# Optimization experiments

Measured on AMD Instinct MI355X. Metric: run time of the kernel, lower is better.

Reference implementation:

```python
import jax, jax.numpy as jnp
import numpy as np

N_HEADS = 16

def setup_inputs() -> dict:
    key = jax.random.key(0)
    qkv = jax.random.normal(key, (4, 3072, 2048), dtype=jnp.float32)
    return {"qkv": qkv}

def reference(qkv) -> jnp.ndarray:
    bs, width, length = qkv.shape
    ch = width // (3 * N_HEADS)
    # [bs*H, 3*ch, T] -> split into q, k, v each [bs*H, ch, T]
    qkv_r = qkv.reshape(bs * N_HEADS, 3 * ch, length)
    q, k, v = qkv_r[:, :ch], qkv_r[:, ch:2 * ch], qkv_r[:, 2 * ch:]
    scale = 1.0 / jnp.sqrt(jnp.sqrt(jnp.float32(ch)))
    # scores: [bs*H, T, T]
    weight = jnp.einsum('bct,bcs->bts', q * scale, k * scale)
    weight = jax.nn.softmax(weight.astype(jnp.float32), axis=-1).astype(weight.dtype)
    a = jnp.einsum('bts,bcs->bct', weight, v)  # [bs*H, ch, T]
    return a.reshape(bs, N_HEADS * ch, length)
```

## Files before the change

### kernel.cpp

```cpp
#include <hip/hip_runtime.h>

namespace {

constexpr int D  = 64;
constexpr int T  = 2048;
constexpr int TQ = 64;
constexpr int NT = T / 64;
constexpr float SCL = 0.125f * 1.44269504088896340736f;

constexpr size_t QP_OFF  = (size_t)64 * 32 * 8192;
constexpr size_t WS_NEED = ((size_t)64 * 32 * 8192 + (size_t)64 * 32 * 4096) * 2;

typedef __bf16 bf16x8 __attribute__((ext_vector_type(8)));
typedef float  f32x4  __attribute__((ext_vector_type(4)));
typedef unsigned short u16x4 __attribute__((ext_vector_type(4)));

__device__ inline unsigned short f2bf(float f) {
    unsigned int u = __builtin_bit_cast(unsigned int, f);
    u += 0x7FFFu + ((u >> 16) & 1u);
    return (unsigned short)(u >> 16);
}

__device__ inline bf16x8 frag8(const unsigned short* p, int row, int c0) {
    int g = (c0 >> 3) ^ ((row >> 1) & 7);
    return *(const bf16x8*)(p + row * 64 + g * 8);
}

__device__ inline void async_cp16(const void* g, void* l) {
    __builtin_amdgcn_global_load_lds(
        (const __attribute__((address_space(1))) unsigned int*)g,
        (__attribute__((address_space(3))) unsigned int*)l, 16, 0, 0);
}

__global__ __launch_bounds__(256)
void prepass(const float* __restrict__ qkv, unsigned short* __restrict__ ws) {
    const int tile = blockIdx.x, h = blockIdx.y, z = blockIdx.z;
    const int tid = threadIdx.x;
    const int c0 = (tid >> 4) * 4;
    const int s4 = tid & 15;
    const float* src = qkv + (size_t)h * 3 * D * T + (size_t)z * D * T + tile * 64;
    unsigned short* dst = (z == 0)
        ? ws + QP_OFF + (size_t)(h * 32 + tile) * 4096
        : ws + (size_t)(h * 32 + tile) * 8192 + (z == 2 ? 4096 : 0);

    float fr[4][4];
    #pragma unroll
    for (int r = 0; r < 4; r++)
        *(f32x4*)fr[r] = *(const f32x4*)(src + (size_t)(c0 + r) * T + s4 * 4);

    if (z < 2) {
        #pragma unroll
        for (int j = 0; j < 4; j++) {
            int trow = s4 * 4 + j;
            int g = (c0 >> 3) ^ ((trow >> 1) & 7);
            u16x4 w = { f2bf(fr[0][j]), f2bf(fr[1][j]), f2bf(fr[2][j]), f2bf(fr[3][j]) };
            *(u16x4*)(dst + trow * 64 + g * 8 + (c0 & 7)) = w;
        }
    } else {
        #pragma unroll
        for (int r = 0; r < 4; r++) {
            int row = c0 + r, cc = s4 * 4;
            int g = (cc >> 3) ^ ((row >> 1) & 7);
            u16x4 w = { f2bf(fr[r][0]), f2bf(fr[r][1]), f2bf(fr[r][2]), f2bf(fr[r][3]) };
            *(u16x4*)(dst + row * 64 + g * 8 + (cc & 7)) = w;
        }
    }
}

__global__ __launch_bounds__(256, 4)
void attn_main(const unsigned short* __restrict__ ws, float* __restrict__ out) {
    const int h  = blockIdx.x;
    const int qt = blockIdx.y;
    const int t0 = qt * TQ;
    const int tid  = threadIdx.x;
    const int lane = tid & 63;
    const int w    = tid >> 6;
    const int sh   = w & 1, th = w >> 1;
    const int ln   = lane & 15, q4 = lane >> 4;

    __shared__ unsigned short KV[2][8192];
    __shared__ unsigned short Ps[4096];

    const unsigned short* qtile = ws + QP_OFF + (size_t)(h * 32 + qt) * 4096;
    bf16x8 bQ[2][2];
    #pragma unroll
    for (int ti = 0; ti < 2; ti++)
        #pragma unroll
        for (int kc = 0; kc < 2; kc++) {
            int t = th * 32 + ti * 16 + ln;
            int g = (kc * 4 + q4) ^ ((t >> 1) & 7);
            bQ[ti][kc] = *(const bf16x8*)(qtile + t * 64 + g * 8);
        }

    const char* kvbase = (const char*)ws + (size_t)(h * 32) * 16384
                         + (size_t)w * 4096 + lane * 16;
    {
        char* l = (char*)&KV[0][0] + w * 4096;
        #pragma unroll
        for (int i = 0; i < 4; i++) async_cp16(kvbase + i * 1024, l + i * 1024);
    }

    f32x4 acc_o[4][2];
    #pragma unroll
    for (int ci = 0; ci < 4; ci++)
        #pragma unroll
        for (int ti = 0; ti < 2; ti++) acc_o[ci][ti] = (f32x4){0.f, 0.f, 0.f, 0.f};
    float l_acc[2] = {0.f, 0.f};

    for (int kt = 0; kt < NT; kt++) {
        const int buf = kt & 1;
        __syncthreads();
        if (kt + 1 < NT) {
            const char* g = kvbase + (size_t)(kt + 1) * 16384;
            char* l = (char*)&KV[buf ^ 1][0] + w * 4096;
            #pragma unroll
            for (int i = 0; i < 4; i++) async_cp16(g + i * 1024, l + i * 1024);
        }
        const unsigned short* Kr = &KV[buf][0];
        const unsigned short* Vr = &KV[buf][4096];

        f32x4 acc_s[2][2];
        #pragma unroll
        for (int si = 0; si < 2; si++)
            #pragma unroll
            for (int ti = 0; ti < 2; ti++) acc_s[si][ti] = (f32x4){0.f, 0.f, 0.f, 0.f};
        #pragma unroll
        for (int kc = 0; kc < 2; kc++)
            #pragma unroll
            for (int si = 0; si < 2; si++) {
                bf16x8 aK = frag8(Kr, sh * 32 + si * 16 + ln, kc * 32 + q4 * 8);
                #pragma unroll
                for (int ti = 0; ti < 2; ti++)
                    acc_s[si][ti] = __builtin_amdgcn_mfma_f32_16x16x32_bf16(
                        aK, bQ[ti][kc], acc_s[si][ti], 0, 0, 0);
            }

        #pragma unroll
        for (int si = 0; si < 2; si++)
            #pragma unroll
            for (int ti = 0; ti < 2; ti++) {
                float p0 = __builtin_amdgcn_exp2f(acc_s[si][ti][0] * SCL);
                float p1 = __builtin_amdgcn_exp2f(acc_s[si][ti][1] * SCL);
                float p2 = __builtin_amdgcn_exp2f(acc_s[si][ti][2] * SCL);
                float p3 = __builtin_amdgcn_exp2f(acc_s[si][ti][3] * SCL);
                l_acc[ti] += (p0 + p1) + (p2 + p3);
                u16x4 pk = { f2bf(p0), f2bf(p1), f2bf(p2), f2bf(p3) };
                int t  = th * 32 + ti * 16 + ln;
                int c0 = sh * 32 + si * 16 + q4 * 4;
                int g  = (c0 >> 3) ^ ((t >> 1) & 7);
                *(u16x4*)(Ps + t * 64 + g * 8 + (c0 & 7)) = pk;
            }

        bf16x8 bP[2];
        #pragma unroll
        for (int ti = 0; ti < 2; ti++)
            bP[ti] = frag8(Ps, th * 32 + ti * 16 + ln, sh * 32 + q4 * 8);
        #pragma unroll
        for (int ci = 0; ci < 4; ci++) {
            bf16x8 aV = frag8(Vr, ci * 16 + ln, sh * 32 + q4 * 8);
            #pragma unroll
            for (int ti = 0; ti < 2; ti++)
                acc_o[ci][ti] = __builtin_amdgcn_mfma_f32_16x16x32_bf16(
                    aV, bP[ti], acc_o[ci][ti], 0, 0, 0);
        }
    }

    __syncthreads();
    float* mrg = (float*)&KV[0][0];
    float* lp  = (float*)Ps;
    #pragma unroll
    for (int ti = 0; ti < 2; ti++) {
        float s = l_acc[ti];
        s += __shfl_xor(s, 16, 64);
        s += __shfl_xor(s, 32, 64);
        if (q4 == 0) lp[th * 64 + sh * 32 + ti * 16 + ln] = s;
    }
    if (sh == 0) {
        float* base = mrg + th * 2048;
        #pragma unroll
        for (int ci = 0; ci < 4; ci++)
            #pragma unroll
            for (int ti = 0; ti < 2; ti++)
                *(f32x4*)(base + (ci * 2 + ti) * 256 + lane * 4) = acc_o[ci][ti];
    }
    __syncthreads();
    if (sh == 1) {
        float* base = mrg + th * 2048;
        float linv[2];
        #pragma unroll
        for (int ti = 0; ti < 2; ti++) {
            int tt = ti * 16 + ln;
            linv[ti] = 1.0f / (lp[th * 64 + tt] + lp[th * 64 + 32 + tt]);
        }
        float* ob = out + (size_t)h * D * T + t0 + th * 32;
        #pragma unroll
        for (int ci = 0; ci < 4; ci++)
            #pragma unroll
            for (int ti = 0; ti < 2; ti++) {
                f32x4 part = *(const f32x4*)(base + (ci * 2 + ti) * 256 + lane * 4);
                #pragma unroll
                for (int r = 0; r < 4; r++) {
                    int c = ci * 16 + q4 * 4 + r;
                    ob[(size_t)c * T + ti * 16 + ln] =
                        (acc_o[ci][ti][r] + part[r]) * linv[ti];
                }
            }
    }
}

__global__ __launch_bounds__(256)
void attn_fallback(const float* __restrict__ qkv, float* __restrict__ out) {
    const int h     = blockIdx.y;
    const int t0    = blockIdx.x * TQ;
    const int tid   = threadIdx.x;
    const int lane  = tid & 63;
    const int strip = tid >> 6;
    const int ln    = lane & 15;
    const int q4    = lane >> 4;

    __shared__ unsigned short Qs[TQ * D];
    __shared__ unsigned short Ks[64 * D];
    __shared__ unsigned short Vs[D * 64];
    __shared__ unsigned short Pss[TQ * 64];
    __shared__ float l_lds[TQ];

    const float* qb = qkv + (size_t)h * 3 * D * T;
    const float* kb = qb + (size_t)D * T;
    const float* vb = qb + (size_t)(2 * D) * T;
    const int s4 = tid & 15;
    const int c0 = (tid >> 4) * 4;
    {
        float fr[4][4];
        #pragma unroll
        for (int r = 0; r < 4; r++)
            *(f32x4*)fr[r] = *(const f32x4*)(qb + (size_t)(c0 + r) * T + t0 + s4 * 4);
        #pragma unroll
        for (int j = 0; j < 4; j++) {
            int trow = s4 * 4 + j;
            int g = (c0 >> 3) ^ ((trow >> 1) & 7);
            u16x4 wv = { f2bf(fr[0][j]), f2bf(fr[1][j]), f2bf(fr[2][j]), f2bf(fr[3][j]) };
            *(u16x4*)(Qs + trow * 64 + g * 8 + (c0 & 7)) = wv;
        }
    }
    __syncthreads();
    const int arow = strip * 16 + ln;
    const int kg   = q4 * 8;
    const bf16x8 aq0 = frag8(Qs, arow, kg);
    const bf16x8 aq1 = frag8(Qs, arow, 32 + kg);
    f32x4 acc_o[4];
    #pragma unroll
    for (int m = 0; m < 4; m++) acc_o[m] = (f32x4){0.f, 0.f, 0.f, 0.f};
    float l_acc[4] = {0.f, 0.f, 0.f, 0.f};
    for (int kt = 0; kt < NT; kt++) {
        const int s0 = kt * 64;
        float kr[4][4], vr[4][4];
        #pragma unroll
        for (int r = 0; r < 4; r++)
            *(f32x4*)kr[r] = *(const f32x4*)(kb + (size_t)(c0 + r) * T + s0 + s4 * 4);
        #pragma unroll
        for (int r = 0; r < 4; r++)
            *(f32x4*)vr[r] = *(const f32x4*)(vb + (size_t)(c0 + r) * T + s0 + s4 * 4);
        __syncthreads();
        #pragma unroll
        for (int j = 0; j < 4; j++) {
            int srow = s4 * 4 + j;
            int g = (c0 >> 3) ^ ((srow >> 1) & 7);
            u16x4 wk = { f2bf(kr[0][j]), f2bf(kr[1][j]), f2bf(kr[2][j]), f2bf(kr[3][j]) };
            *(u16x4*)(Ks + srow * 64 + g * 8 + (c0 & 7)) = wk;
        }
        #pragma unroll
        for (int r = 0; r < 4; r++) {
            int row = c0 + r, cc = s4 * 4;
            int g = (cc >> 3) ^ ((row >> 1) & 7);
            u16x4 wv = { f2bf(vr[r][0]), f2bf(vr[r][1]), f2bf(vr[r][2]), f2bf(vr[r][3]) };
            *(u16x4*)(Vs + row * 64 + g * 8 + (cc & 7)) = wv;
        }
        __syncthreads();
        f32x4 accs[4];
        #pragma unroll
        for (int ns = 0; ns < 4; ns++) {
            bf16x8 b0 = frag8(Ks, ns * 16 + ln, kg);
            bf16x8 b1 = frag8(Ks, ns * 16 + ln, 32 + kg);
            f32x4 z = {0.f, 0.f, 0.f, 0.f};
            z = __builtin_amdgcn_mfma_f32_16x16x32_bf16(aq0, b0, z, 0, 0, 0);
            z = __builtin_amdgcn_mfma_f32_16x16x32_bf16(aq1, b1, z, 0, 0, 0);
            accs[ns] = z;
        }
        #pragma unroll
        for (int ns = 0; ns < 4; ns++) {
            int scol = ns * 16 + ln;
            #pragma unroll
            for (int r = 0; r < 4; r++) {
                float p = __builtin_amdgcn_exp2f(accs[ns][r] * SCL);
                l_acc[r] += p;
                int trow = strip * 16 + q4 * 4 + r;
                int g = ((scol >> 3) ^ ((trow >> 1) & 7));
                Pss[trow * 64 + g * 8 + (scol & 7)] = f2bf(p);
            }
        }
        bf16x8 bp0 = frag8(Pss, arow, kg);
        bf16x8 bp1 = frag8(Pss, arow, 32 + kg);
        #pragma unroll
        for (int ms = 0; ms < 4; ms++) {
            bf16x8 av0 = frag8(Vs, ms * 16 + ln, kg);
            bf16x8 av1 = frag8(Vs, ms * 16 + ln, 32 + kg);
            acc_o[ms] = __builtin_amdgcn_mfma_f32_16x16x32_bf16(av0, bp0, acc_o[ms], 0, 0, 0);
            acc_o[ms] = __builtin_amdgcn_mfma_f32_16x16x32_bf16(av1, bp1, acc_o[ms], 0, 0, 0);
        }
    }
    #pragma unroll
    for (int r = 0; r < 4; r++) {
        float s = l_acc[r];
        s += __shfl_xor(s, 1, 64);
        s += __shfl_xor(s, 2, 64);
        s += __shfl_xor(s, 4, 64);
        s += __shfl_xor(s, 8, 64);
        if (ln == 0) l_lds[strip * 16 + q4 * 4 + r] = s;
    }
    const float linv = 1.0f / l_lds[strip * 16 + ln];
    const int tg = t0 + strip * 16 + ln;
    float* ob = out + (size_t)h * D * T;
    #pragma unroll
    for (int ms = 0; ms < 4; ms++)
        #pragma unroll
        for (int r = 0; r < 4; r++) {
            int c = ms * 16 + q4 * 4 + r;
            ob[(size_t)c * T + tg] = acc_o[ms][r] * linv;
        }
}

}

extern "C" void kernel_launch(void* const* d_in, const int* in_sizes, int n_in,
                              void* d_out, int out_size, void* d_ws, size_t ws_size,
                              hipStream_t stream) {
    const float* qkv = (const float*)d_in[0];
    float* out = (float*)d_out;
    if (ws_size >= WS_NEED) {
        prepass<<<dim3(32, 64, 3), 256, 0, stream>>>(qkv, (unsigned short*)d_ws);
        attn_main<<<dim3(64, 32), 256, 0, stream>>>((const unsigned short*)d_ws, out);
    } else {
        attn_fallback<<<dim3(32, 64), 256, 0, stream>>>(qkv, out);
    }
}
```

Baseline: 257.7 us.

## Fold softmax scale into Q prepass, precompute LDS pointers, unroll KV loop by two

```diff
diff --git a/kernel.cpp b/kernel.cpp
--- a/kernel.cpp
+++ b/kernel.cpp
@@ -14,6 +14,7 @@
 typedef __bf16 bf16x8 __attribute__((ext_vector_type(8)));
 typedef float  f32x4  __attribute__((ext_vector_type(4)));
 typedef unsigned short u16x4 __attribute__((ext_vector_type(4)));
+typedef unsigned short u16x8 __attribute__((ext_vector_type(8)));
 
 __device__ inline unsigned short f2bf(float f) {
     unsigned int u = __builtin_bit_cast(unsigned int, f);
@@ -21,9 +22,9 @@
     return (unsigned short)(u >> 16);
 }
 
-__device__ inline bf16x8 frag8(const unsigned short* p, int row, int c0) {
+__device__ inline int frag_off(int row, int c0) {
     int g = (c0 >> 3) ^ ((row >> 1) & 7);
-    return *(const bf16x8*)(p + row * 64 + g * 8);
+    return row * 64 + g * 8;
 }
 
 __device__ inline void async_cp16(const void* g, void* l) {
@@ -36,36 +37,99 @@
 void prepass(const float* __restrict__ qkv, unsigned short* __restrict__ ws) {
     const int tile = blockIdx.x, h = blockIdx.y, z = blockIdx.z;
     const int tid = threadIdx.x;
-    const int c0 = (tid >> 4) * 4;
-    const int s4 = tid & 15;
     const float* src = qkv + (size_t)h * 3 * D * T + (size_t)z * D * T + tile * 64;
-    unsigned short* dst = (z == 0)
-        ? ws + QP_OFF + (size_t)(h * 32 + tile) * 4096
-        : ws + (size_t)(h * 32 + tile) * 8192 + (z == 2 ? 4096 : 0);
-
-    float fr[4][4];
-    #pragma unroll
-    for (int r = 0; r < 4; r++)
-        *(f32x4*)fr[r] = *(const f32x4*)(src + (size_t)(c0 + r) * T + s4 * 4);
-
-    if (z < 2) {
+    __shared__ unsigned short L[4096];
+
+    if (z == 2) {
+        unsigned short* dst = ws + (size_t)(h * 32 + tile) * 8192 + 4096;
+        #pragma unroll
+        for (int half = 0; half < 2; half++) {
+            int idx = half * 256 + tid;
+            int row = idx >> 3, g = idx & 7;
+            int gg  = g ^ ((row >> 1) & 7);
+            f32x4 a = *(const f32x4*)(src + (size_t)row * T + gg * 8);
+            f32x4 b = *(const f32x4*)(src + (size_t)row * T + gg * 8 + 4);
+            u16x8 wv = { f2bf(a[0]), f2bf(a[1]), f2bf(a[2]), f2bf(a[3]),
+                         f2bf(b[0]), f2bf(b[1]), f2bf(b[2]), f2bf(b[3]) };
+            *(u16x8*)(dst + idx * 8) = wv;
+        }
+    } else {
+        const float m = (z == 0) ? SCL : 1.0f;
+        const int c0 = (tid >> 4) * 4, s4 = tid & 15;
+        float fr[4][4];
+        #pragma unroll
+        for (int r = 0; r < 4; r++)
+            *(f32x4*)fr[r] = *(const f32x4*)(src + (size_t)(c0 + r) * T + s4 * 4);
         #pragma unroll
         for (int j = 0; j < 4; j++) {
             int trow = s4 * 4 + j;
-            int g = (c0 >> 3) ^ ((trow >> 1) & 7);
-            u16x4 w = { f2bf(fr[0][j]), f2bf(fr[1][j]), f2bf(fr[2][j]), f2bf(fr[3][j]) };
-            *(u16x4*)(dst + trow * 64 + g * 8 + (c0 & 7)) = w;
-        }
-    } else {
-        #pragma unroll
-        for (int r = 0; r < 4; r++) {
-            int row = c0 + r, cc = s4 * 4;
-            int g = (cc >> 3) ^ ((row >> 1) & 7);
-            u16x4 w = { f2bf(fr[r][0]), f2bf(fr[r][1]), f2bf(fr[r][2]), f2bf(fr[r][3]) };
-            *(u16x4*)(dst + row * 64 + g * 8 + (cc & 7)) = w;
-        }
-    }
-}
+            u16x4 wv = { f2bf(fr[0][j] * m), f2bf(fr[1][j] * m),
+                         f2bf(fr[2][j] * m), f2bf(fr[3][j] * m) };
+            *(u16x4*)(L + frag_off(trow, c0) + (c0 & 7)) = wv;
+        }
+        __syncthreads();
+        unsigned short* dst = (z == 0)
+            ? ws + QP_OFF + (size_t)(h * 32 + tile) * 4096
+            : ws + (size_t)(h * 32 + tile) * 8192;
+        #pragma unroll
+        for (int i = 0; i < 2; i++)
+            *(u16x8*)(dst + tid * 16 + i * 8) =
+                *(const u16x8*)(L + tid * 16 + i * 8);
+    }
+}
+
+
+#define ATTN_BODY(KT, B)                                                      \
+  {                                                                           \
+    const int kt_ = (KT);                                                     \
+    __syncthreads();   \
+    if (kt_ < NT - 1) {                                                       \
+      const char* gsrc = kvbase + (size_t)(kt_ + 1) * 16384;                  \
+      _Pragma("unroll")                                                       \
+      for (int i = 0; i < 4; i++)                                             \
+        async_cp16(gsrc + i * 1024, stage[(B) ^ 1] + i * 1024);               \
+    }                                                                         \
+    f32x4 acc_s[2][2];                                                        \
+    _Pragma("unroll")                                                         \
+    for (int si = 0; si < 2; si++)                                            \
+      _Pragma("unroll")                                                       \
+      for (int ti = 0; ti < 2; ti++)                                          \
+        acc_s[si][ti] = (f32x4){0.f, 0.f, 0.f, 0.f};                          \
+    _Pragma("unroll")                                                         \
+    for (int kc = 0; kc < 2; kc++)                                            \
+      _Pragma("unroll")                                                       \
+      for (int si = 0; si < 2; si++) {                                        \
+        bf16x8 aK = *(const bf16x8*)aKp[B][kc][si];                           \
+        _Pragma("unroll")                                                     \
+        for (int ti = 0; ti < 2; ti++)                                        \
+          acc_s[si][ti] = __builtin_amdgcn_mfma_f32_16x16x32_bf16(            \
+              aK, bQ[ti][kc], acc_s[si][ti], 0, 0, 0);                        \
+      }                                                                       \
+                 \
+    _Pragma("unroll")                                                         \
+    for (int si = 0; si < 2; si++)                                            \
+      _Pragma("unroll")                                                       \
+      for (int ti = 0; ti < 2; ti++) {                                        \
+        float p0 = __builtin_amdgcn_exp2f(acc_s[si][ti][0]);                  \
+        float p1 = __builtin_amdgcn_exp2f(acc_s[si][ti][1]);                  \
+        float p2 = __builtin_amdgcn_exp2f(acc_s[si][ti][2]);                  \
+        float p3 = __builtin_amdgcn_exp2f(acc_s[si][ti][3]);                  \
+        l_acc[ti] += (p0 + p1) + (p2 + p3);                                   \
+        u16x4 pk = { f2bf(p0), f2bf(p1), f2bf(p2), f2bf(p3) };                \
+        *(u16x4*)pwp[si][ti] = pk;                                            \
+      }                                                                       \
+          \
+    bf16x8 bP0 = *(const bf16x8*)bPp[0];                                      \
+    bf16x8 bP1 = *(const bf16x8*)bPp[1];                                      \
+    _Pragma("unroll")                                                         \
+    for (int ci = 0; ci < 4; ci++) {                                          \
+      bf16x8 aV = *(const bf16x8*)aVp[B][ci];                                 \
+      acc_o[ci][0] = __builtin_amdgcn_mfma_f32_16x16x32_bf16(                 \
+          aV, bP0, acc_o[ci][0], 0, 0, 0);                                    \
+      acc_o[ci][1] = __builtin_amdgcn_mfma_f32_16x16x32_bf16(                 \
+          aV, bP1, acc_o[ci][1], 0, 0, 0);                                    \
+    }                                                                         \
+  }
 
 __global__ __launch_bounds__(256, 4)
 void attn_main(const unsigned short* __restrict__ ws, float* __restrict__ out) {
@@ -88,17 +152,42 @@
         #pragma unroll
         for (int kc = 0; kc < 2; kc++) {
             int t = th * 32 + ti * 16 + ln;
-            int g = (kc * 4 + q4) ^ ((t >> 1) & 7);
-            bQ[ti][kc] = *(const bf16x8*)(qtile + t * 64 + g * 8);
-        }
+            bQ[ti][kc] = *(const bf16x8*)(qtile + frag_off(t, kc * 32 + q4 * 8));
+        }
+
+    const unsigned short* aKp[2][2][2];
+    const unsigned short* aVp[2][4];
+    const unsigned short* bPp[2];
+    unsigned short*       pwp[2][2];
+    char*                 stage[2];
+    #pragma unroll
+    for (int b = 0; b < 2; b++) {
+        const unsigned short* Kr = &KV[b][0];
+        const unsigned short* Vr = &KV[b][4096];
+        #pragma unroll
+        for (int kc = 0; kc < 2; kc++)
+            #pragma unroll
+            for (int si = 0; si < 2; si++)
+                aKp[b][kc][si] = Kr + frag_off(sh * 32 + si * 16 + ln, kc * 32 + q4 * 8);
+        #pragma unroll
+        for (int ci = 0; ci < 4; ci++)
+            aVp[b][ci] = Vr + frag_off(ci * 16 + ln, sh * 32 + q4 * 8);
+        stage[b] = (char*)&KV[b][0] + w * 4096;
+    }
+    #pragma unroll
+    for (int ti = 0; ti < 2; ti++) {
+        bPp[ti] = Ps + frag_off(th * 32 + ti * 16 + ln, sh * 32 + q4 * 8);
+        #pragma unroll
+        for (int si = 0; si < 2; si++) {
+            int t = th * 32 + ti * 16 + ln, c0p = sh * 32 + si * 16 + q4 * 4;
+            pwp[si][ti] = Ps + frag_off(t, c0p) + (c0p & 7);
+        }
+    }
 
     const char* kvbase = (const char*)ws + (size_t)(h * 32) * 16384
                          + (size_t)w * 4096 + lane * 16;
-    {
-        char* l = (char*)&KV[0][0] + w * 4096;
-        #pragma unroll
-        for (int i = 0; i < 4; i++) async_cp16(kvbase + i * 1024, l + i * 1024);
-    }
+    #pragma unroll
+    for (int i = 0; i < 4; i++) async_cp16(kvbase + i * 1024, stage[0] + i * 1024);
 
     f32x4 acc_o[4][2];
     #pragma unroll
@@ -107,62 +196,10 @@
         for (int ti = 0; ti < 2; ti++) acc_o[ci][ti] = (f32x4){0.f, 0.f, 0.f, 0.f};
     float l_acc[2] = {0.f, 0.f};
 
-    for (int kt = 0; kt < NT; kt++) {
-        const int buf = kt & 1;
-        __syncthreads();
-        if (kt + 1 < NT) {
-            const char* g = kvbase + (size_t)(kt + 1) * 16384;
-            char* l = (char*)&KV[buf ^ 1][0] + w * 4096;
-            #pragma unroll
-            for (int i = 0; i < 4; i++) async_cp16(g + i * 1024, l + i * 1024);
-        }
-        const unsigned short* Kr = &KV[buf][0];
-        const unsigned short* Vr = &KV[buf][4096];
-
-        f32x4 acc_s[2][2];
-        #pragma unroll
-        for (int si = 0; si < 2; si++)
-            #pragma unroll
-            for (int ti = 0; ti < 2; ti++) acc_s[si][ti] = (f32x4){0.f, 0.f, 0.f, 0.f};
-        #pragma unroll
-        for (int kc = 0; kc < 2; kc++)
-            #pragma unroll
-            for (int si = 0; si < 2; si++) {
-                bf16x8 aK = frag8(Kr, sh * 32 + si * 16 + ln, kc * 32 + q4 * 8);
-                #pragma unroll
-                for (int ti = 0; ti < 2; ti++)
-                    acc_s[si][ti] = __builtin_amdgcn_mfma_f32_16x16x32_bf16(
-                        aK, bQ[ti][kc], acc_s[si][ti], 0, 0, 0);
-            }
-
-        #pragma unroll
-        for (int si = 0; si < 2; si++)
-            #pragma unroll
-            for (int ti = 0; ti < 2; ti++) {
-                float p0 = __builtin_amdgcn_exp2f(acc_s[si][ti][0] * SCL);
-                float p1 = __builtin_amdgcn_exp2f(acc_s[si][ti][1] * SCL);
-                float p2 = __builtin_amdgcn_exp2f(acc_s[si][ti][2] * SCL);
-                float p3 = __builtin_amdgcn_exp2f(acc_s[si][ti][3] * SCL);
-                l_acc[ti] += (p0 + p1) + (p2 + p3);
-                u16x4 pk = { f2bf(p0), f2bf(p1), f2bf(p2), f2bf(p3) };
-                int t  = th * 32 + ti * 16 + ln;
-                int c0 = sh * 32 + si * 16 + q4 * 4;
-                int g  = (c0 >> 3) ^ ((t >> 1) & 7);
-                *(u16x4*)(Ps + t * 64 + g * 8 + (c0 & 7)) = pk;
-            }
-
-        bf16x8 bP[2];
-        #pragma unroll
-        for (int ti = 0; ti < 2; ti++)
-            bP[ti] = frag8(Ps, th * 32 + ti * 16 + ln, sh * 32 + q4 * 8);
-        #pragma unroll
-        for (int ci = 0; ci < 4; ci++) {
-            bf16x8 aV = frag8(Vr, ci * 16 + ln, sh * 32 + q4 * 8);
-            #pragma unroll
-            for (int ti = 0; ti < 2; ti++)
-                acc_o[ci][ti] = __builtin_amdgcn_mfma_f32_16x16x32_bf16(
-                    aV, bP[ti], acc_o[ci][ti], 0, 0, 0);
-        }
+    #pragma unroll 1
+    for (int m = 0; m < NT / 2; m++) {
+        ATTN_BODY(2 * m,     0)
+        ATTN_BODY(2 * m + 1, 1)
     }
 
     __syncthreads();
@@ -208,6 +245,10 @@
     }
 }
 
+__device__ inline bf16x8 frag8(const unsigned short* p, int row, int c0) {
+    return *(const bf16x8*)(p + frag_off(row, c0));
+}
+
 __global__ __launch_bounds__(256)
 void attn_fallback(const float* __restrict__ qkv, float* __restrict__ out) {
     const int h     = blockIdx.y;
@@ -237,9 +278,8 @@
         #pragma unroll
         for (int j = 0; j < 4; j++) {
             int trow = s4 * 4 + j;
-            int g = (c0 >> 3) ^ ((trow >> 1) & 7);
             u16x4 wv = { f2bf(fr[0][j]), f2bf(fr[1][j]), f2bf(fr[2][j]), f2bf(fr[3][j]) };
-            *(u16x4*)(Qs + trow * 64 + g * 8 + (c0 & 7)) = wv;
+            *(u16x4*)(Qs + frag_off(trow, c0) + (c0 & 7)) = wv;
         }
     }
     __syncthreads();
@@ -251,6 +291,7 @@
     #pragma unroll
     for (int m = 0; m < 4; m++) acc_o[m] = (f32x4){0.f, 0.f, 0.f, 0.f};
     float l_acc[4] = {0.f, 0.f, 0.f, 0.f};
+    constexpr float S2 = 0.125f * 1.44269504088896340736f;
     for (int kt = 0; kt < NT; kt++) {
         const int s0 = kt * 64;
         float kr[4][4], vr[4][4];
@@ -264,16 +305,14 @@
         #pragma unroll
         for (int j = 0; j < 4; j++) {
             int srow = s4 * 4 + j;
-            int g = (c0 >> 3) ^ ((srow >> 1) & 7);
             u16x4 wk = { f2bf(kr[0][j]), f2bf(kr[1][j]), f2bf(kr[2][j]), f2bf(kr[3][j]) };
-            *(u16x4*)(Ks + srow * 64 + g * 8 + (c0 & 7)) = wk;
+            *(u16x4*)(Ks + frag_off(srow, c0) + (c0 & 7)) = wk;
         }
         #pragma unroll
         for (int r = 0; r < 4; r++) {
             int row = c0 + r, cc = s4 * 4;
-            int g = (cc >> 3) ^ ((row >> 1) & 7);
             u16x4 wv = { f2bf(vr[r][0]), f2bf(vr[r][1]), f2bf(vr[r][2]), f2bf(vr[r][3]) };
-            *(u16x4*)(Vs + row * 64 + g * 8 + (cc & 7)) = wv;
+            *(u16x4*)(Vs + frag_off(row, cc) + (cc & 7)) = wv;
         }
         __syncthreads();
         f32x4 accs[4];
@@ -291,7 +330,7 @@
             int scol = ns * 16 + ln;
             #pragma unroll
             for (int r = 0; r < 4; r++) {
-                float p = __builtin_amdgcn_exp2f(accs[ns][r] * SCL);
+                float p = __builtin_amdgcn_exp2f(accs[ns][r] * S2);
                 l_acc[r] += p;
                 int trow = strip * 16 + q4 * 4 + r;
                 int g = ((scol >> 3) ^ ((trow >> 1) & 7));
```

Measured after the change: 255.7 us. Within noise of the previous version (-0.8%).
